# Kernel tuning notes

Hardware: AMD Instinct MI355X
Metric: run time of the kernel (lower is better)

## Reference

```python
import jax, jax.numpy as jnp
import numpy as np

B, L, H, D, VOC, C, P = 16, 256, 6, 768, 32000, 20, 1
d = D // H
MAXF = 20
BN_EPS = 1e-5


def setup_inputs() -> dict:
    key = jax.random.key(0)
    ks = jax.random.split(key, 8)
    doc_tids = jax.random.randint(ks[0], (B, L), 0, VOC)
    TFs = jax.random.uniform(ks[1], (B, L), dtype=jnp.float32) * 20.0 + 1.0
    DFs = jax.random.uniform(ks[2], (B, L), dtype=jnp.float32) * 1000.0 + 1.0
    emb = jax.random.normal(ks[3], (VOC, D), dtype=jnp.float32) * 0.02
    fcW = jax.random.normal(ks[4], (C + P, D), dtype=jnp.float32) * 0.02
    fcb = jnp.zeros((C + P,), dtype=jnp.float32)
    weiW = jax.random.normal(ks[5], (2, H), dtype=jnp.float32) * 0.1
    weib = jnp.zeros((2,), dtype=jnp.float32)
    return dict(doc_tids=doc_tids, TFs=TFs, DFs=DFs, emb=emb,
                fcW=fcW, fcb=fcb, weiW=weiW, weib=weib)


def _bn(x):
    # BatchNorm over channel axis 1 (H), batch stats over all other axes (train mode, affine=False)
    m = x.mean(axis=(0, 2, 3), keepdims=True)
    v = x.var(axis=(0, 2, 3), keepdims=True)
    return (x - m) * jax.lax.rsqrt(v + BN_EPS)


def _leaky9(x):
    return jnp.where(x >= 0, x, 9.0 * x)


def reference(doc_tids, TFs, DFs, emb, fcW, fcb, weiW, weib):
    # --- EmbbedingTFIDF (eval mode, dropout off): tf-idf weighted embedding lookup ---
    tf = jnp.minimum(TFs, float(MAXF))
    idf = jnp.log1p(1.0 / DFs)
    x = emb[doc_tids] * (tf * idf)[:, :, None]          # (B, L, D)
    valid = doc_tids != 0
    # model flips pad_mask with logical_not, then co_weights[pad_mask] = 0
    invalid = ~(valid[:, :, None] & valid[:, None, :])  # (B, L, L) True -> zero out
    mask = invalid[:, None, :, :]                       # broadcast over heads

    def split_heads(h):
        return h.reshape(B, L, H, d).transpose(0, 2, 1, 3)  # (B, H, L, d)

    Q = split_heads(x)
    K = Q
    V = Q

    # --- nearAttention (layers=1) ---
    Vn = _bn(V)
    # DistMatrix: pairwise Euclidean distance dist[b,h,i,j] = ||K_i - Q_j||
    Ksq = jnp.sum(K * K, axis=-1)[..., :, None]
    Qsq = jnp.sum(Q * Q, axis=-1)[..., None, :]
    cross = jnp.einsum('bhid,bhjd->bhij', K, Q)
    co = jnp.sqrt(jnp.maximum(Ksq + Qsq - 2.0 * cross, 1e-12))  # (B, H, L, L)
    # BatchNorm1d(H) over flattened (B, H, L*L) == per-H stats over (0,2,3)
    co = _leaky9(_bn(co))
    co = jnp.where(mask, 0.0, co)
    co = jax.nn.softmax(co, axis=-1)
    co = jnp.where(jnp.isnan(co), 0.0, co)
    V_out = jnp.einsum('bhij,bhjd->bhid', co, Vn)
    Q_out = _bn(jnp.einsum('bhij,bhjd->bhid', co, Q))
    K_out = _bn(jnp.einsum('bhij,bhjd->bhid', co, K))

    # --- head ---
    Vc = V_out.transpose(0, 2, 1, 3).reshape(B, L, D)       # catHiddens
    V_lgts = jax.nn.softmax(Vc @ fcW.T + fcb, axis=-1)      # (B, L, C+P)
    cw = jnp.swapaxes(co, -1, -2).reshape(B, L * L, H)      # transpose then contiguous reshape
    cw = jax.nn.softmax(cw @ weiW.T + weib, axis=-1)        # (B, L*L, 2)
    cw = cw.reshape(B, L, L, 2).sum(axis=-2, keepdims=True)[:, :, :, 0]  # (B, L, 1)
    cw = jax.nn.softmax(cw, axis=-1)                        # softmax over singleton -> ones (faithful)
    logits = (cw * V_lgts).sum(axis=1)[:, :C]               # (B, C)
    logits = jax.nn.softmax(logits, axis=-1)
    return logits
```

## Files before the change

kernel.cpp:

```cpp
#include <hip/hip_runtime.h>
#include <hip/hip_bf16.h>
#include <math.h>

#define OFF_XT   1572864UL
#define OFF_VC   3145728UL
#define OFF_SQ   4718592UL
#define OFF_PART 4767744UL
#define OFF_ACC  4780056UL
#define OFF_CTR  4780392UL
#define OFF_FCWB 4780396UL
#define OFF_CV   8388608UL

typedef __attribute__((ext_vector_type(8))) __bf16 bf16x8;
typedef __attribute__((ext_vector_type(4))) float f32x4;
typedef __attribute__((ext_vector_type(8))) unsigned short u16x8;

__global__ __launch_bounds__(512) void k12_fused(const int* __restrict__ tids,
    const float* __restrict__ TF, const float* __restrict__ DF,
    const float* __restrict__ emb, unsigned short* __restrict__ xT,
    float* __restrict__ sq, float* __restrict__ part, const float* __restrict__ fcW,
    unsigned short* __restrict__ fcWb, float* __restrict__ acc,
    unsigned int* __restrict__ ctr, float* __restrict__ cvws) {
  int bid = blockIdx.x;
  int xcd = bid & 7, idx = bid >> 3;
  int bh = xcd * 12 + idx % 12;
  int jq = idx / 12;
  int b = bh / 6, h = bh % 6;
  int tid = threadIdx.x;
  __shared__ unsigned short tile[32768];
  __shared__ float swd1[8], swd2[8], swv1[8], swv2[8];
  if (jq == 1) {
    if (tid < 168) {
      int i2 = bh * 168 + tid;
      fcWb[i2] = __bfloat16_as_ushort(__float2bfloat16(fcW[i2]));
    }
  } else if (jq == 0 && bh == 0) {
    if (tid < 336) acc[tid] = 0.0f;
    if (tid == 336) *ctr = 0u;
  }
  int sub = tid & 7, row0 = tid >> 3;
  int c16 = sub * 16;
  float ts1 = 0.0f, ts2 = 0.0f;
#pragma unroll
  for (int p = 0; p < 4; ++p) {
    int r = p * 64 + row0;
    int tok = b * 256 + r;
    int tv = tids[tok];
    float wgt = fminf(TF[tok], 20.0f) * log1pf(1.0f / DF[tok]);
    const float* er = emb + (size_t)tv * 768 + h * 128 + c16;
    float4 e0 = *(const float4*)er;
    float4 e1 = *(const float4*)(er + 4);
    float4 e2 = *(const float4*)(er + 8);
    float4 e3 = *(const float4*)(er + 12);
    float f[16] = {e0.x, e0.y, e0.z, e0.w, e1.x, e1.y, e1.z, e1.w,
                   e2.x, e2.y, e2.z, e2.w, e3.x, e3.y, e3.z, e3.w};
    u16x8 pk0, pk1;
    float s1 = 0.0f, s2 = 0.0f;
#pragma unroll
    for (int e = 0; e < 8; ++e) {
      __hip_bfloat16 hb = __float2bfloat16(f[e] * wgt);
      float g = __bfloat162float(hb);
      s1 += g; s2 += g * g;
      pk0[e] = __bfloat16_as_ushort(hb);
    }
#pragma unroll
    for (int e = 0; e < 8; ++e) {
      __hip_bfloat16 hb = __float2bfloat16(f[8 + e] * wgt);
      float g = __bfloat162float(hb);
      s1 += g; s2 += g * g;
      pk1[e] = __bfloat16_as_ushort(hb);
    }
    ts1 += s1; ts2 += s2;
    int rx = r & 7;
    *(u16x8*)&tile[r * 128 + (((sub * 2    ) ^ rx) * 8)] = pk0;
    *(u16x8*)&tile[r * 128 + (((sub * 2 + 1) ^ rx) * 8)] = pk1;
    s2 += __shfl_down(s2, 4); s2 += __shfl_down(s2, 2); s2 += __shfl_down(s2, 1);
    if (sub == 0)
      sq[(size_t)bh * 256 + r] = s2;
  }
  __syncthreads();
  if (jq == 3) {
    int ch = tid & 127, q = tid >> 7;
    int cc = ch >> 3, cs = ch & 7;
    unsigned int* xo = (unsigned int*)xT + ((size_t)bh * 128 + ch) * 128 + q * 32;
#pragma unroll
    for (int g = 0; g < 8; ++g) {
      unsigned int tmp[4];
#pragma unroll
      for (int k = 0; k < 4; ++k) {
        int t0 = q * 64 + (g * 4 + k) * 2;
        unsigned int lo = tile[ t0      * 128 + ((cc ^ ( t0      & 7)) * 8) + cs];
        unsigned int hi = tile[(t0 + 1) * 128 + ((cc ^ ((t0 + 1) & 7)) * 8) + cs];
        tmp[k] = lo | (hi << 16);
      }
      uint4 vv; vv.x = tmp[0]; vv.y = tmp[1]; vv.z = tmp[2]; vv.w = tmp[3];
      *(uint4*)(xo + g * 4) = vv;
    }
  }
  int w = tid >> 6, lane = tid & 63, quad = lane >> 4, l16 = lane & 15;
  const float* sqh = sq + (size_t)bh * 256;
  int it0 = w * 2;
  bf16x8 a2[2][4];
  float si2[2][4];
#pragma unroll
  for (int ith = 0; ith < 2; ++ith) {
    int ar = (it0 + ith) * 16 + l16, arx = ar & 7;
#pragma unroll
    for (int k0 = 0; k0 < 4; ++k0)
      a2[ith][k0] = *(const bf16x8*)&tile[ar * 128 + (((k0 * 4 + quad) ^ arx) * 8)];
#pragma unroll
    for (int r = 0; r < 4; ++r)
      si2[ith][r] = sqh[(it0 + ith) * 16 + quad * 4 + r];
  }
  float ls1 = 0.0f, ls2 = 0.0f;
#pragma unroll
  for (int jt = 0; jt < 4; ++jt) {
    int jcol = jq * 64 + jt * 16 + l16;
    int jrx = jcol & 7;
    bf16x8 bfr[4];
#pragma unroll
    for (int k0 = 0; k0 < 4; ++k0)
      bfr[k0] = *(const bf16x8*)&tile[jcol * 128 + (((k0 * 4 + quad) ^ jrx) * 8)];
    f32x4 acc0 = {0.0f, 0.0f, 0.0f, 0.0f}, acc1 = {0.0f, 0.0f, 0.0f, 0.0f};
#pragma unroll
    for (int k0 = 0; k0 < 4; ++k0) {
      acc0 = __builtin_amdgcn_mfma_f32_16x16x32_bf16(a2[0][k0], bfr[k0], acc0, 0, 0, 0);
      acc1 = __builtin_amdgcn_mfma_f32_16x16x32_bf16(a2[1][k0], bfr[k0], acc1, 0, 0, 0);
    }
    float sj = sqh[jcol];
#pragma unroll
    for (int r = 0; r < 4; ++r) {
      float cv0 = sqrtf(fmaxf(si2[0][r] + sj - 2.0f * acc0[r], 1e-12f));
      float cv1 = sqrtf(fmaxf(si2[1][r] + sj - 2.0f * acc1[r], 1e-12f));
      cvws[((size_t)bh * 256 + (it0    ) * 16 + quad * 4 + r) * 256 + jcol] = cv0;
      cvws[((size_t)bh * 256 + (it0 + 1) * 16 + quad * 4 + r) * 256 + jcol] = cv1;
      ls1 += cv0 + cv1;
      ls2 += cv0 * cv0 + cv1 * cv1;
    }
  }
#pragma unroll
  for (int off = 32; off >= 1; off >>= 1) {
    ls1 += __shfl_down(ls1, off);
    ls2 += __shfl_down(ls2, off);
    ts1 += __shfl_down(ts1, off);
    ts2 += __shfl_down(ts2, off);
  }
  if (lane == 0) { swd1[w] = ls1; swd2[w] = ls2; swv1[w] = ts1; swv2[w] = ts2; }
  __syncthreads();
  if (tid == 0) {
    float d1 = 0.0f, d2 = 0.0f, v1 = 0.0f, v2 = 0.0f;
#pragma unroll
    for (int i = 0; i < 8; ++i) { d1 += swd1[i]; d2 += swd2[i]; v1 += swv1[i]; v2 += swv2[i]; }
    part[192 + (bh * 4 + jq) * 2 + 0] = d1;
    part[192 + (bh * 4 + jq) * 2 + 1] = d2;
    if (jq == 0) { part[bh * 2] = v1; part[bh * 2 + 1] = v2; }
  }
}

__global__ __launch_bounds__(256) void k45_fused(const float* __restrict__ cvws,
    const unsigned short* __restrict__ xT, const int* __restrict__ tids,
    const float* __restrict__ part, unsigned short* __restrict__ vc16) {
  int bid = blockIdx.x;
  int xcd = bid & 7, idx = bid >> 3;
  int bh = xcd * 12 + idx % 12;
  int p = idx / 12;
  int b = bh / 6, h = bh % 6;
  int tid = threadIdx.x, w = tid >> 6, lane = tid & 63;
  int quad = lane >> 4, l16 = lane & 15;
  int I = p * 16;
  __shared__ float scv[16][257];
  __shared__ float svld[256];
  __shared__ unsigned short cot[16][264];
  __shared__ float smax[16][4];
  __shared__ float ssum[16][4];
  __shared__ float sstat[4];
  svld[tid] = (tids[b * 256 + tid] != 0) ? 1.0f : 0.0f;
  {
    int row = tid >> 4, cseg = (tid & 15) * 16;
    const float* src = cvws + ((size_t)bh * 256 + I + row) * 256 + cseg;
    float4 v0 = *(const float4*)src;
    float4 v1 = *(const float4*)(src + 4);
    float4 v2 = *(const float4*)(src + 8);
    float4 v3 = *(const float4*)(src + 12);
    *(float4*)&scv[row][cseg + 0]  = v0;
    *(float4*)&scv[row][cseg + 4]  = v1;
    *(float4*)&scv[row][cseg + 8]  = v2;
    *(float4*)&scv[row][cseg + 12] = v3;
  }
  if (w == 0) {
    float c1 = 0.0f, c2 = 0.0f;
    {
      int bb = lane >> 2, jj = lane & 3;
      c1 = part[192 + ((bb * 6 + h) * 4 + jj) * 2 + 0];
      c2 = part[192 + ((bb * 6 + h) * 4 + jj) * 2 + 1];
    }
    float v1 = 0.0f, v2 = 0.0f;
    if (lane < 16) {
      v1 = part[(lane * 6 + h) * 2 + 0];
      v2 = part[(lane * 6 + h) * 2 + 1];
    }
#pragma unroll
    for (int off = 32; off >= 1; off >>= 1) {
      c1 += __shfl_down(c1, off);
      c2 += __shfl_down(c2, off);
      v1 += __shfl_down(v1, off);
      v2 += __shfl_down(v2, off);
    }
    if (lane == 0) {
      float mean = c1 / 1048576.0f;
      float var = c2 / 1048576.0f - mean * mean;
      sstat[0] = mean;
      sstat[1] = rsqrtf(var + 1e-5f);
      float mv = v1 / 524288.0f;
      float vv = v2 / 524288.0f - mv * mv;
      sstat[2] = mv;
      sstat[3] = rsqrtf(vv + 1e-5f);
    }
  }
  __syncthreads();
  float m = sstat[0], rsc = sstat[1];
  float rv[4];
#pragma unroll
  for (int r = 0; r < 4; ++r) rv[r] = svld[I + quad * 4 + r];
  float y[4][4];
#pragma unroll
  for (int tl = 0; tl < 4; ++tl) {
    int t = w * 4 + tl;
    float cvld = svld[t * 16 + l16];
#pragma unroll
    for (int r = 0; r < 4; ++r) {
      float cv = scv[quad * 4 + r][t * 16 + l16];
      float yv = (cv - m) * rsc;
      yv = yv >= 0.0f ? yv : 9.0f * yv;
      y[tl][r] = yv * rv[r] * cvld;
    }
  }
#pragma unroll
  for (int r = 0; r < 4; ++r) {
    float mx = fmaxf(fmaxf(y[0][r], y[1][r]), fmaxf(y[2][r], y[3][r]));
#pragma unroll
    for (int off = 1; off <= 8; off <<= 1) mx = fmaxf(mx, __shfl_xor(mx, off));
    if (l16 == 0) smax[quad * 4 + r][w] = mx;
  }
  __syncthreads();
  float gmx[4];
#pragma unroll
  for (int r = 0; r < 4; ++r) {
    int row = quad * 4 + r;
    gmx[r] = fmaxf(fmaxf(smax[row][0], smax[row][1]), fmaxf(smax[row][2], smax[row][3]));
    float s = 0.0f;
#pragma unroll
    for (int tl = 0; tl < 4; ++tl) { y[tl][r] = expf(y[tl][r] - gmx[r]); s += y[tl][r]; }
#pragma unroll
    for (int off = 1; off <= 8; off <<= 1) s += __shfl_xor(s, off);
    if (l16 == 0) ssum[row][w] = s;
  }
  __syncthreads();
#pragma unroll
  for (int r = 0; r < 4; ++r) {
    int row = quad * 4 + r;
    float gs = ssum[row][0] + ssum[row][1] + ssum[row][2] + ssum[row][3];
    float inv = 1.0f / gs;
#pragma unroll
    for (int tl = 0; tl < 4; ++tl)
      cot[row][w * 64 + tl * 16 + l16] =
          __bfloat16_as_ushort(__float2bfloat16(y[tl][r] * inv));
  }
  __syncthreads();
  bf16x8 a2[8];
#pragma unroll
  for (int k0 = 0; k0 < 8; ++k0)
    a2[k0] = *(const bf16x8*)&cot[l16][k0 * 32 + quad * 8];
  __syncthreads();
  const __bf16* xbT = (const __bf16*)xT + (size_t)bh * 128 * 256;
  float mv = sstat[2], rvs = sstat[3];
  float rm = rvs * mv;
#pragma unroll
  for (int jl = 0; jl < 2; ++jl) {
    int ch = (w * 2 + jl) * 16 + l16;
    const __bf16* brow = xbT + (size_t)ch * 256;
    f32x4 vacc = {0.0f, 0.0f, 0.0f, 0.0f};
#pragma unroll
    for (int k0 = 0; k0 < 8; ++k0) {
      bf16x8 bfr = *(const bf16x8*)(brow + k0 * 32 + quad * 8);
      vacc = __builtin_amdgcn_mfma_f32_16x16x32_bf16(a2[k0], bfr, vacc, 0, 0, 0);
    }
#pragma unroll
    for (int r = 0; r < 4; ++r) {
      float ov = rvs * vacc[r] - rm;
      cot[quad * 4 + r][ch] = __bfloat16_as_ushort(__float2bfloat16(ov));
    }
  }
  __syncthreads();
  {
    int row = tid >> 4, seg = (tid & 15) * 8;
    u16x8 pkv = *(const u16x8*)&cot[row][seg];
    *(u16x8*)(vc16 + ((size_t)(b * 256 + I + row)) * 768 + h * 128 + seg) = pkv;
  }
}

__global__ __launch_bounds__(256) void k5b6_lgts(const unsigned short* __restrict__ vc16,
    const unsigned short* __restrict__ fcWb, const float* __restrict__ fcb,
    float* __restrict__ acc, unsigned int* __restrict__ ctr, float* __restrict__ out) {
  int bid = blockIdx.x;
  int xcd = bid & 7, idx = bid >> 3;
  int b = xcd * 2 + (idx & 1);
  int qa = idx >> 1;
  int tid = threadIdx.x, w = tid >> 6, lane = tid & 63;
  int quad = lane >> 4, l16 = lane & 15;
  int tok0 = b * 256 + qa * 64 + w * 16;
  int c1c = (l16 < 5) ? (16 + l16) : 20;
  const __bf16* vb = (const __bf16*)vc16;
  const __bf16* w0 = (const __bf16*)fcWb + (size_t)l16 * 768;
  const __bf16* w1 = (const __bf16*)fcWb + (size_t)c1c * 768;
  f32x4 ac0 = {0.0f, 0.0f, 0.0f, 0.0f}, ac1 = {0.0f, 0.0f, 0.0f, 0.0f};
#pragma unroll
  for (int k0 = 0; k0 < 24; ++k0) {
    int ko = k0 * 32 + quad * 8;
    bf16x8 af = *(const bf16x8*)(vb + (size_t)(tok0 + l16) * 768 + ko);
    bf16x8 b0 = *(const bf16x8*)(w0 + ko);
    bf16x8 b1 = *(const bf16x8*)(w1 + ko);
    ac0 = __builtin_amdgcn_mfma_f32_16x16x32_bf16(af, b0, ac0, 0, 0, 0);
    ac1 = __builtin_amdgcn_mfma_f32_16x16x32_bf16(af, b1, ac1, 0, 0, 0);
  }
  float bias0 = fcb[l16];
  float bias1 = (l16 < 5) ? fcb[16 + l16] : 0.0f;
  float p0s = 0.0f, p1s = 0.0f;
#pragma unroll
  for (int r = 0; r < 4; ++r) {
    float lg0 = ac0[r] + bias0;
    float lg1 = (l16 < 5) ? (ac1[r] + bias1) : -1e30f;
    float mx = fmaxf(lg0, lg1);
#pragma unroll
    for (int off = 1; off <= 8; off <<= 1) mx = fmaxf(mx, __shfl_xor(mx, off));
    float e0 = expf(lg0 - mx), e1 = expf(lg1 - mx);
    float s = e0 + e1;
#pragma unroll
    for (int off = 1; off <= 8; off <<= 1) s += __shfl_xor(s, off);
    float inv = 1.0f / s;
    p0s += e0 * inv;
    p1s += e1 * inv;
  }
  p0s += __shfl_xor(p0s, 16); p0s += __shfl_xor(p0s, 32);
  p1s += __shfl_xor(p1s, 16); p1s += __shfl_xor(p1s, 32);
  __shared__ float sacc[4][21];
  __shared__ unsigned int sdone;
  if (quad == 0) sacc[w][l16] = p0s;
  if (quad == 1 && l16 < 5) sacc[w][16 + l16] = p1s;
  __syncthreads();
  if (tid < 21) {
    float s = sacc[0][tid] + sacc[1][tid] + sacc[2][tid] + sacc[3][tid];
    atomicAdd(&acc[b * 21 + tid], s);
  }
  __syncthreads();
  if (tid == 0) {
    __threadfence();
    sdone = atomicAdd(ctr, 1u);
  }
  __syncthreads();
  if (sdone == 63u && tid < 16) {
    float v[20];
    float mx = -1e30f;
#pragma unroll
    for (int c = 0; c < 20; ++c) {
      v[c] = atomicAdd(&acc[tid * 21 + c], 0.0f);
      mx = fmaxf(mx, v[c]);
    }
    float s = 0.0f;
#pragma unroll
    for (int c = 0; c < 20; ++c) { v[c] = expf(v[c] - mx); s += v[c]; }
    float inv = 1.0f / s;
#pragma unroll
    for (int c = 0; c < 20; ++c) out[tid * 20 + c] = v[c] * inv;
  }
}

extern "C" void kernel_launch(void* const* d_in, const int* in_sizes, int n_in,
                              void* d_out, int out_size, void* d_ws, size_t ws_size,
                              hipStream_t stream) {
  const int*   tids = (const int*)d_in[0];
  const float* TF   = (const float*)d_in[1];
  const float* DF   = (const float*)d_in[2];
  const float* emb  = (const float*)d_in[3];
  const float* fcW  = (const float*)d_in[4];
  const float* fcb  = (const float*)d_in[5];
  float* out = (float*)d_out;
  float* ws  = (float*)d_ws;
  unsigned short* xT   = (unsigned short*)(ws + OFF_XT);
  unsigned short* vc   = (unsigned short*)(ws + OFF_VC);
  unsigned short* fcWb = (unsigned short*)(ws + OFF_FCWB);
  float* sq    = ws + OFF_SQ;
  float* part  = ws + OFF_PART;
  float* acc   = ws + OFF_ACC;
  float* cvws  = ws + OFF_CV;
  unsigned int* ctr = (unsigned int*)(ws + OFF_CTR);

  k12_fused<<<384, 512, 0, stream>>>(tids, TF, DF, emb, xT, sq, part,
                                     fcW, fcWb, acc, ctr, cvws);
  k45_fused<<<1536, 256, 0, stream>>>(cvws, xT, tids, part, vc);
  k5b6_lgts<<<64, 256, 0, stream>>>(vc, fcWb, fcb, acc, ctr, out);
}
```

Measured before the change: 186.6 us.

## Reassociate V_out and fc projection: precompute X·Wᵀ per head, apply co to projections

Because the fc layer is linear and the V batch-norm is affine per head, the logits equal rvs·(co·(X·W_hᵀ)) minus a per-head mean correction plus bias. The first kernel now computes the 21-column per-head projection of the embeddings and row sums of fcW. The attention kernel multiplies co by this small projection and accumulates per-token logits atomically instead of producing the full 768-wide V_out. This removes the transposed X copy, the wide co·V MFMA, and the bf16 V_out round-trip. In exchange it adds atomics and a change in bf16 rounding order.

```diff
diff --git a/kernel.cpp b/kernel.cpp
--- a/kernel.cpp
+++ b/kernel.cpp
@@ -2,25 +2,27 @@
 #include <hip/hip_bf16.h>
 #include <math.h>
 
-#define OFF_XT   1572864UL
-#define OFF_VC   3145728UL
-#define OFF_SQ   4718592UL
-#define OFF_PART 4767744UL
-#define OFF_ACC  4780056UL
-#define OFF_CTR  4780392UL
-#define OFF_FCWB 4780396UL
-#define OFF_CV   8388608UL
+#define OFF_GRAWT 1572864UL
+#define OFF_LGACC 3145728UL
+#define OFF_SQ    4718592UL
+#define OFF_PART  4767744UL
+#define OFF_ACC   4780056UL
+#define OFF_CTR   4780392UL
+#define OFF_W1S   4780396UL
+#define OFF_CV    8388608UL
 
 typedef __attribute__((ext_vector_type(8))) __bf16 bf16x8;
 typedef __attribute__((ext_vector_type(4))) float f32x4;
 typedef __attribute__((ext_vector_type(8))) unsigned short u16x8;
+typedef __attribute__((ext_vector_type(4))) unsigned short u16x4;
 
 __global__ __launch_bounds__(512) void k12_fused(const int* __restrict__ tids,
     const float* __restrict__ TF, const float* __restrict__ DF,
-    const float* __restrict__ emb, unsigned short* __restrict__ xT,
-    float* __restrict__ sq, float* __restrict__ part, const float* __restrict__ fcW,
-    unsigned short* __restrict__ fcWb, float* __restrict__ acc,
-    unsigned int* __restrict__ ctr, float* __restrict__ cvws) {
+    const float* __restrict__ emb, float* __restrict__ sq,
+    float* __restrict__ part, const float* __restrict__ fcW,
+    float* __restrict__ W1s, float* __restrict__ lgacc, float* __restrict__ acc,
+    unsigned int* __restrict__ ctr, float* __restrict__ cvws,
+    unsigned short* __restrict__ grawt) {
   int bid = blockIdx.x;
   int xcd = bid & 7, idx = bid >> 3;
   int bh = xcd * 12 + idx % 12;
@@ -29,12 +31,18 @@
   int tid = threadIdx.x;
   __shared__ unsigned short tile[32768];
   __shared__ float swd1[8], swd2[8], swv1[8], swv2[8];
-  if (jq == 1) {
-    if (tid < 168) {
-      int i2 = bh * 168 + tid;
-      fcWb[i2] = __bfloat16_as_ushort(__float2bfloat16(fcW[i2]));
-    }
-  } else if (jq == 0 && bh == 0) {
+  {
+    float* lz = lgacc + (size_t)bid * 224;
+    for (int i = tid; i < 224; i += 512) lz[i] = 0.0f;
+  }
+  if (jq == 1 && bh == 0 && tid < 126) {
+    int hh = tid / 21, c = tid % 21;
+    const float* fr = fcW + (size_t)c * 768 + hh * 128;
+    float s = 0.0f;
+    for (int k = 0; k < 128; ++k) s += fr[k];
+    W1s[tid] = s;
+  }
+  if (jq == 0 && bh == 0) {
     if (tid < 336) acc[tid] = 0.0f;
     if (tid == 336) *ctr = 0u;
   }
@@ -79,24 +87,6 @@
       sq[(size_t)bh * 256 + r] = s2;
   }
   __syncthreads();
-  if (jq == 3) {
-    int ch = tid & 127, q = tid >> 7;
-    int cc = ch >> 3, cs = ch & 7;
-    unsigned int* xo = (unsigned int*)xT + ((size_t)bh * 128 + ch) * 128 + q * 32;
-#pragma unroll
-    for (int g = 0; g < 8; ++g) {
-      unsigned int tmp[4];
-#pragma unroll
-      for (int k = 0; k < 4; ++k) {
-        int t0 = q * 64 + (g * 4 + k) * 2;
-        unsigned int lo = tile[ t0      * 128 + ((cc ^ ( t0      & 7)) * 8) + cs];
-        unsigned int hi = tile[(t0 + 1) * 128 + ((cc ^ ((t0 + 1) & 7)) * 8) + cs];
-        tmp[k] = lo | (hi << 16);
-      }
-      uint4 vv; vv.x = tmp[0]; vv.y = tmp[1]; vv.z = tmp[2]; vv.w = tmp[3];
-      *(uint4*)(xo + g * 4) = vv;
-    }
-  }
   int w = tid >> 6, lane = tid & 63, quad = lane >> 4, l16 = lane & 15;
   const float* sqh = sq + (size_t)bh * 256;
   int it0 = w * 2;
@@ -138,6 +128,28 @@
       ls2 += cv0 * cv0 + cv1 * cv1;
     }
   }
+  {
+    int jt = w >> 1, ct = w & 1;
+    int jrow = jq * 64 + jt * 16 + l16, jrx = jrow & 7;
+    int cc = ct * 16 + l16; if (cc > 20) cc = 20;
+    const float* fwr = fcW + (size_t)cc * 768 + h * 128;
+    f32x4 ga = {0.0f, 0.0f, 0.0f, 0.0f};
+#pragma unroll
+    for (int k0 = 0; k0 < 4; ++k0) {
+      bf16x8 af = *(const bf16x8*)&tile[jrow * 128 + (((k0 * 4 + quad) ^ jrx) * 8)];
+      const float* bp = fwr + k0 * 32 + quad * 8;
+      u16x8 bb;
+#pragma unroll
+      for (int e = 0; e < 8; ++e) bb[e] = __bfloat16_as_ushort(__float2bfloat16(bp[e]));
+      ga = __builtin_amdgcn_mfma_f32_16x16x32_bf16(af, *(const bf16x8*)&bb, ga, 0, 0, 0);
+    }
+    if (ct == 0 || l16 < 5) {
+      u16x4 pk;
+#pragma unroll
+      for (int r = 0; r < 4; ++r) pk[r] = __bfloat16_as_ushort(__float2bfloat16(ga[r]));
+      *(u16x4*)(grawt + ((size_t)bh * 21 + ct * 16 + l16) * 256 + jq * 64 + jt * 16 + quad * 4) = pk;
+    }
+  }
 #pragma unroll
   for (int off = 32; off >= 1; off >>= 1) {
     ls1 += __shfl_down(ls1, off);
@@ -158,8 +170,8 @@
 }
 
 __global__ __launch_bounds__(256) void k45_fused(const float* __restrict__ cvws,
-    const unsigned short* __restrict__ xT, const int* __restrict__ tids,
-    const float* __restrict__ part, unsigned short* __restrict__ vc16) {
+    const unsigned short* __restrict__ grawt, const int* __restrict__ tids,
+    const float* __restrict__ part, float* __restrict__ lgacc) {
   int bid = blockIdx.x;
   int xcd = bid & 7, idx = bid >> 3;
   int bh = xcd * 12 + idx % 12;
@@ -174,6 +186,11 @@
   __shared__ float smax[16][4];
   __shared__ float ssum[16][4];
   __shared__ float sstat[4];
+  __shared__ float sacc[16][21];
+  if (tid < 168) {
+    ((float*)sacc)[tid] = 0.0f;
+    ((float*)sacc)[tid + 168] = 0.0f;
+  }
   svld[tid] = (tids[b * 256 + tid] != 0) ? 1.0f : 0.0f;
   {
     int row = tid >> 4, cseg = (tid & 15) * 16;
@@ -267,111 +284,102 @@
           __bfloat16_as_ushort(__float2bfloat16(y[tl][r] * inv));
   }
   __syncthreads();
-  bf16x8 a2[8];
-#pragma unroll
-  for (int k0 = 0; k0 < 8; ++k0)
-    a2[k0] = *(const bf16x8*)&cot[l16][k0 * 32 + quad * 8];
-  __syncthreads();
-  const __bf16* xbT = (const __bf16*)xT + (size_t)bh * 128 * 256;
-  float mv = sstat[2], rvs = sstat[3];
-  float rm = rvs * mv;
-#pragma unroll
-  for (int jl = 0; jl < 2; ++jl) {
-    int ch = (w * 2 + jl) * 16 + l16;
-    const __bf16* brow = xbT + (size_t)ch * 256;
-    f32x4 vacc = {0.0f, 0.0f, 0.0f, 0.0f};
-#pragma unroll
-    for (int k0 = 0; k0 < 8; ++k0) {
-      bf16x8 bfr = *(const bf16x8*)(brow + k0 * 32 + quad * 8);
-      vacc = __builtin_amdgcn_mfma_f32_16x16x32_bf16(a2[k0], bfr, vacc, 0, 0, 0);
-    }
-#pragma unroll
-    for (int r = 0; r < 4; ++r) {
-      float ov = rvs * vacc[r] - rm;
-      cot[quad * 4 + r][ch] = __bfloat16_as_ushort(__float2bfloat16(ov));
-    }
-  }
-  __syncthreads();
   {
-    int row = tid >> 4, seg = (tid & 15) * 8;
-    u16x8 pkv = *(const u16x8*)&cot[row][seg];
-    *(u16x8*)(vc16 + ((size_t)(b * 256 + I + row)) * 768 + h * 128 + seg) = pkv;
+    bf16x8 pa0 = *(const bf16x8*)&cot[l16][(w * 2 + 0) * 32 + quad * 8];
+    bf16x8 pa1 = *(const bf16x8*)&cot[l16][(w * 2 + 1) * 32 + quad * 8];
+#pragma unroll
+    for (int ct = 0; ct < 2; ++ct) {
+      int cc = ct * 16 + l16;
+      bool cval = (cc < 21);
+      int ccl = cval ? cc : 20;
+      const __bf16* gb = (const __bf16*)grawt + ((size_t)bh * 21 + ccl) * 256;
+      f32x4 pacc = {0.0f, 0.0f, 0.0f, 0.0f};
+      pacc = __builtin_amdgcn_mfma_f32_16x16x32_bf16(
+          pa0, *(const bf16x8*)(gb + (w * 2 + 0) * 32 + quad * 8), pacc, 0, 0, 0);
+      pacc = __builtin_amdgcn_mfma_f32_16x16x32_bf16(
+          pa1, *(const bf16x8*)(gb + (w * 2 + 1) * 32 + quad * 8), pacc, 0, 0, 0);
+      if (cval) {
+#pragma unroll
+        for (int r = 0; r < 4; ++r) atomicAdd(&sacc[quad * 4 + r][cc], pacc[r]);
+      }
+    }
+  }
+  __syncthreads();
+  float rvs = sstat[3];
+  for (int e = tid; e < 336; e += 256) {
+    int i = e / 21, c = e % 21;
+    atomicAdd(&lgacc[((size_t)b * 256 + I + i) * 21 + c], rvs * sacc[i][c]);
   }
 }
 
-__global__ __launch_bounds__(256) void k5b6_lgts(const unsigned short* __restrict__ vc16,
-    const unsigned short* __restrict__ fcWb, const float* __restrict__ fcb,
-    float* __restrict__ acc, unsigned int* __restrict__ ctr, float* __restrict__ out) {
-  int bid = blockIdx.x;
-  int xcd = bid & 7, idx = bid >> 3;
-  int b = xcd * 2 + (idx & 1);
-  int qa = idx >> 1;
+__global__ __launch_bounds__(256) void k5b6_lgts(const float* __restrict__ lgacc,
+    const float* __restrict__ part, const float* __restrict__ W1s,
+    const float* __restrict__ fcb, float* __restrict__ acc,
+    unsigned int* __restrict__ ctr, float* __restrict__ out) {
+  int b = blockIdx.x;
   int tid = threadIdx.x, w = tid >> 6, lane = tid & 63;
-  int quad = lane >> 4, l16 = lane & 15;
-  int tok0 = b * 256 + qa * 64 + w * 16;
-  int c1c = (l16 < 5) ? (16 + l16) : 20;
-  const __bf16* vb = (const __bf16*)vc16;
-  const __bf16* w0 = (const __bf16*)fcWb + (size_t)l16 * 768;
-  const __bf16* w1 = (const __bf16*)fcWb + (size_t)c1c * 768;
-  f32x4 ac0 = {0.0f, 0.0f, 0.0f, 0.0f}, ac1 = {0.0f, 0.0f, 0.0f, 0.0f};
-#pragma unroll
-  for (int k0 = 0; k0 < 24; ++k0) {
-    int ko = k0 * 32 + quad * 8;
-    bf16x8 af = *(const bf16x8*)(vb + (size_t)(tok0 + l16) * 768 + ko);
-    bf16x8 b0 = *(const bf16x8*)(w0 + ko);
-    bf16x8 b1 = *(const bf16x8*)(w1 + ko);
-    ac0 = __builtin_amdgcn_mfma_f32_16x16x32_bf16(af, b0, ac0, 0, 0, 0);
-    ac1 = __builtin_amdgcn_mfma_f32_16x16x32_bf16(af, b1, ac1, 0, 0, 0);
-  }
-  float bias0 = fcb[l16];
-  float bias1 = (l16 < 5) ? fcb[16 + l16] : 0.0f;
-  float p0s = 0.0f, p1s = 0.0f;
-#pragma unroll
-  for (int r = 0; r < 4; ++r) {
-    float lg0 = ac0[r] + bias0;
-    float lg1 = (l16 < 5) ? (ac1[r] + bias1) : -1e30f;
-    float mx = fmaxf(lg0, lg1);
-#pragma unroll
-    for (int off = 1; off <= 8; off <<= 1) mx = fmaxf(mx, __shfl_xor(mx, off));
-    float e0 = expf(lg0 - mx), e1 = expf(lg1 - mx);
-    float s = e0 + e1;
-#pragma unroll
-    for (int off = 1; off <= 8; off <<= 1) s += __shfl_xor(s, off);
-    float inv = 1.0f / s;
-    p0s += e0 * inv;
-    p1s += e1 * inv;
-  }
-  p0s += __shfl_xor(p0s, 16); p0s += __shfl_xor(p0s, 32);
-  p1s += __shfl_xor(p1s, 16); p1s += __shfl_xor(p1s, 32);
-  __shared__ float sacc[4][21];
+  __shared__ float sv1[96], sv2[96];
+  __shared__ float sst[6][2];
+  __shared__ float sC[21];
+  __shared__ float wsum[4][21];
   __shared__ unsigned int sdone;
-  if (quad == 0) sacc[w][l16] = p0s;
-  if (quad == 1 && l16 < 5) sacc[w][16 + l16] = p1s;
+  if (tid < 96) { sv1[tid] = part[tid * 2]; sv2[tid] = part[tid * 2 + 1]; }
+  __syncthreads();
+  if (tid < 6) {
+    float v1 = 0.0f, v2 = 0.0f;
+#pragma unroll
+    for (int bb = 0; bb < 16; ++bb) { v1 += sv1[bb * 6 + tid]; v2 += sv2[bb * 6 + tid]; }
+    float mv = v1 / 524288.0f;
+    float vv = v2 / 524288.0f - mv * mv;
+    sst[tid][0] = mv;
+    sst[tid][1] = rsqrtf(vv + 1e-5f);
+  }
   __syncthreads();
   if (tid < 21) {
-    float s = sacc[0][tid] + sacc[1][tid] + sacc[2][tid] + sacc[3][tid];
-    atomicAdd(&acc[b * 21 + tid], s);
-  }
-  __syncthreads();
-  if (tid == 0) {
-    __threadfence();
-    sdone = atomicAdd(ctr, 1u);
-  }
-  __syncthreads();
-  if (sdone == 63u && tid < 16) {
+    float C = 0.0f;
+#pragma unroll
+    for (int hh = 0; hh < 6; ++hh) C += sst[hh][1] * sst[hh][0] * W1s[hh * 21 + tid];
+    sC[tid] = fcb[tid] - C;
+  }
+  __syncthreads();
+  const float* lgr = lgacc + ((size_t)b * 256 + tid) * 21;
+  float lg[21];
+  float mx = -1e30f;
+#pragma unroll
+  for (int c = 0; c < 21; ++c) { lg[c] = lgr[c] + sC[c]; mx = fmaxf(mx, lg[c]); }
+  float s = 0.0f;
+#pragma unroll
+  for (int c = 0; c < 21; ++c) { lg[c] = expf(lg[c] - mx); s += lg[c]; }
+  float inv = 1.0f / s;
+#pragma unroll
+  for (int c = 0; c < 21; ++c) {
+    float v = lg[c] * inv;
+    v += __shfl_down(v, 32); v += __shfl_down(v, 16); v += __shfl_down(v, 8);
+    v += __shfl_down(v, 4);  v += __shfl_down(v, 2);  v += __shfl_down(v, 1);
+    if (lane == 0) wsum[w][c] = v;
+  }
+  __syncthreads();
+  if (tid < 21) {
+    float sv = wsum[0][tid] + wsum[1][tid] + wsum[2][tid] + wsum[3][tid];
+    atomicAdd(&acc[b * 21 + tid], sv);
+  }
+  __syncthreads();
+  if (tid == 0) { __threadfence(); sdone = atomicAdd(ctr, 1u); }
+  __syncthreads();
+  if (sdone == 15u && tid < 16) {
     float v[20];
-    float mx = -1e30f;
+    float mx2 = -1e30f;
 #pragma unroll
     for (int c = 0; c < 20; ++c) {
       v[c] = atomicAdd(&acc[tid * 21 + c], 0.0f);
-      mx = fmaxf(mx, v[c]);
-    }
-    float s = 0.0f;
-#pragma unroll
-    for (int c = 0; c < 20; ++c) { v[c] = expf(v[c] - mx); s += v[c]; }
-    float inv = 1.0f / s;
-#pragma unroll
-    for (int c = 0; c < 20; ++c) out[tid * 20 + c] = v[c] * inv;
+      mx2 = fmaxf(mx2, v[c]);
+    }
+    float s2 = 0.0f;
+#pragma unroll
+    for (int c = 0; c < 20; ++c) { v[c] = expf(v[c] - mx2); s2 += v[c]; }
+    float inv2 = 1.0f / s2;
+#pragma unroll
+    for (int c = 0; c < 20; ++c) out[tid * 20 + c] = v[c] * inv2;
   }
 }
 
@@ -386,17 +394,17 @@
   const float* fcb  = (const float*)d_in[5];
   float* out = (float*)d_out;
   float* ws  = (float*)d_ws;
-  unsigned short* xT   = (unsigned short*)(ws + OFF_XT);
-  unsigned short* vc   = (unsigned short*)(ws + OFF_VC);
-  unsigned short* fcWb = (unsigned short*)(ws + OFF_FCWB);
+  unsigned short* grawt = (unsigned short*)(ws + OFF_GRAWT);
+  float* lgacc = ws + OFF_LGACC;
   float* sq    = ws + OFF_SQ;
   float* part  = ws + OFF_PART;
   float* acc   = ws + OFF_ACC;
+  float* W1s   = ws + OFF_W1S;
   float* cvws  = ws + OFF_CV;
   unsigned int* ctr = (unsigned int*)(ws + OFF_CTR);
 
-  k12_fused<<<384, 512, 0, stream>>>(tids, TF, DF, emb, xT, sq, part,
-                                     fcW, fcWb, acc, ctr, cvws);
-  k45_fused<<<1536, 256, 0, stream>>>(cvws, xT, tids, part, vc);
-  k5b6_lgts<<<64, 256, 0, stream>>>(vc, fcWb, fcb, acc, ctr, out);
+  k12_fused<<<384, 512, 0, stream>>>(tids, TF, DF, emb, sq, part, fcW,
+                                     W1s, lgacc, acc, ctr, cvws, grawt);
+  k45_fused<<<1536, 256, 0, stream>>>(cvws, grawt, tids, part, lgacc);
+  k5b6_lgts<<<16, 256, 0, stream>>>(lgacc, part, W1s, fcb, acc, ctr, out);
 }
```

New measurement: 193.9 us. +3.9%, slower.
